# Kernel tuning notes

Hardware: AMD Instinct MI355X
Metric: run time of the kernel (lower is better)

The kernel has to match this reference:

```python
import jax, jax.numpy as jnp
import numpy as np

NUM_LAYERS, B, S, H = 2, 32, 4096, 1024
NEG_INF = -1.0e9


def setup_inputs() -> dict:
    key = jax.random.key(0)
    k1, k2, k3 = jax.random.split(key, 3)
    hidden = jax.random.normal(k1, (NUM_LAYERS, B, H), dtype=jnp.float32)
    encoder_outputs = jax.random.normal(k2, (B, S, H), dtype=jnp.float32)
    mask = jax.random.randint(k3, (B, S), 0, 2).astype(jnp.bool_)
    return {"hidden": hidden, "encoder_outputs": encoder_outputs, "mask": mask}


def reference(hidden, encoder_outputs, mask):
    # hidden: [L, B, H] -> take last layer [B, H]
    h = hidden[-1]
    # scores: [B, S] = einsum over H
    scores = jnp.einsum("bsh,bh->bs", encoder_outputs, h)
    scores = jnp.where(mask, scores, NEG_INF)
    attn = jax.nn.softmax(scores, axis=1)  # [B, S]
    # context: [B, H]
    context = jnp.einsum("bs,bsh->bh", attn, encoder_outputs)
    return (context, attn)
```

## Files before the change

kernel.cpp:

```cpp
#include <hip/hip_runtime.h>
#include <math.h>

#define B_ 32
#define S_ 4096
#define H_ 1024
#define NBLK 16
#define ROWS_PER_BLOCK (S_ / NBLK)
#define NWAVE 4
#define ROWS_PER_WAVE (ROWS_PER_BLOCK / NWAVE)
#define NEG_INF_ -1.0e9f

__global__ __launch_bounds__(256) void attn_pass1(
    const float* __restrict__ hidden,
    const float* __restrict__ enc,
    const int*   __restrict__ mask,
    float* __restrict__ scores,
    float* __restrict__ part_ctx,
    float* __restrict__ part_ml)
{
    const int blk  = blockIdx.x;
    const int b    = blk / NBLK;
    const int cb   = blk % NBLK;
    const int tid  = threadIdx.x;
    const int wave = tid >> 6;
    const int lane = tid & 63;

    const float4* h4 = (const float4*)(hidden + (size_t)(B_ + b) * H_);
    const float4 hf0 = h4[lane];
    const float4 hf1 = h4[lane + 64];
    const float4 hf2 = h4[lane + 128];
    const float4 hf3 = h4[lane + 192];

    float m = -INFINITY;
    float l = 0.0f;
    float4 c0 = {0.f, 0.f, 0.f, 0.f};
    float4 c1 = c0, c2 = c0, c3 = c0;
    float myscore = 0.0f;

    const int    row0  = cb * ROWS_PER_BLOCK + wave * ROWS_PER_WAVE;
    const float* encb  = enc  + (size_t)b * S_ * H_;
    const int*   maskb = mask + (size_t)b * S_;

    for (int r = 0; r < ROWS_PER_WAVE; ++r) {
        const int s = row0 + r;
        const float4* row4 = (const float4*)(encb + (size_t)s * H_);
        const float4 r0 = row4[lane];
        const float4 r1 = row4[lane + 64];
        const float4 r2 = row4[lane + 128];
        const float4 r3 = row4[lane + 192];

        float dot = r0.x * hf0.x + r0.y * hf0.y + r0.z * hf0.z + r0.w * hf0.w;
        dot += r1.x * hf1.x + r1.y * hf1.y + r1.z * hf1.z + r1.w * hf1.w;
        dot += r2.x * hf2.x + r2.y * hf2.y + r2.z * hf2.z + r2.w * hf2.w;
        dot += r3.x * hf3.x + r3.y * hf3.y + r3.z * hf3.z + r3.w * hf3.w;

        #pragma unroll
        for (int off = 32; off >= 1; off >>= 1)
            dot += __shfl_xor(dot, off, 64);

        const float score = (maskb[s] != 0) ? dot : NEG_INF_;
        if (r == lane) myscore = score;

        const float newm  = fmaxf(m, score);
        const float scale = __expf(m - newm);
        const float p     = __expf(score - newm);
        l = l * scale + p;
        c0.x = c0.x * scale + p * r0.x;  c0.y = c0.y * scale + p * r0.y;
        c0.z = c0.z * scale + p * r0.z;  c0.w = c0.w * scale + p * r0.w;
        c1.x = c1.x * scale + p * r1.x;  c1.y = c1.y * scale + p * r1.y;
        c1.z = c1.z * scale + p * r1.z;  c1.w = c1.w * scale + p * r1.w;
        c2.x = c2.x * scale + p * r2.x;  c2.y = c2.y * scale + p * r2.y;
        c2.z = c2.z * scale + p * r2.z;  c2.w = c2.w * scale + p * r2.w;
        c3.x = c3.x * scale + p * r3.x;  c3.y = c3.y * scale + p * r3.y;
        c3.z = c3.z * scale + p * r3.z;  c3.w = c3.w * scale + p * r3.w;
        m = newm;
    }

    scores[(size_t)b * S_ + row0 + lane] = myscore;

    __shared__ float lds_ctx[NWAVE][H_];
    __shared__ float lds_m[NWAVE];
    __shared__ float lds_l[NWAVE];
    float4* dst = (float4*)lds_ctx[wave];
    dst[lane]       = c0;
    dst[lane + 64]  = c1;
    dst[lane + 128] = c2;
    dst[lane + 192] = c3;
    if (lane == 0) { lds_m[wave] = m; lds_l[wave] = l; }
    __syncthreads();

    const float M  = fmaxf(fmaxf(lds_m[0], lds_m[1]), fmaxf(lds_m[2], lds_m[3]));
    const float w0 = __expf(lds_m[0] - M);
    const float w1 = __expf(lds_m[1] - M);
    const float w2 = __expf(lds_m[2] - M);
    const float w3 = __expf(lds_m[3] - M);

    const int e = tid * 4;
    const float4 a0 = *(const float4*)&lds_ctx[0][e];
    const float4 a1 = *(const float4*)&lds_ctx[1][e];
    const float4 a2 = *(const float4*)&lds_ctx[2][e];
    const float4 a3 = *(const float4*)&lds_ctx[3][e];
    float4 o;
    o.x = a0.x * w0 + a1.x * w1 + a2.x * w2 + a3.x * w3;
    o.y = a0.y * w0 + a1.y * w1 + a2.y * w2 + a3.y * w3;
    o.z = a0.z * w0 + a1.z * w1 + a2.z * w2 + a3.z * w3;
    o.w = a0.w * w0 + a1.w * w1 + a2.w * w2 + a3.w * w3;
    *(float4*)&part_ctx[(size_t)blk * H_ + e] = o;

    if (tid == 0) {
        const float L = lds_l[0] * w0 + lds_l[1] * w1 + lds_l[2] * w2 + lds_l[3] * w3;
        part_ml[blk * 2]     = M;
        part_ml[blk * 2 + 1] = L;
    }
}

__global__ __launch_bounds__(256) void attn_pass2(
    const float* __restrict__ part_ctx,
    const float* __restrict__ part_ml,
    float* __restrict__ out_ctx,
    float* __restrict__ attn)
{
    const int b    = blockIdx.x;
    const int part = blockIdx.y;
    const int tid  = threadIdx.x;

    float M = -INFINITY;
    #pragma unroll
    for (int p = 0; p < NBLK; ++p)
        M = fmaxf(M, part_ml[(b * NBLK + p) * 2]);

    float w[NBLK];
    float L = 0.0f;
    #pragma unroll
    for (int p = 0; p < NBLK; ++p) {
        w[p] = __expf(part_ml[(b * NBLK + p) * 2] - M);
        L += part_ml[(b * NBLK + p) * 2 + 1] * w[p];
    }
    const float invL = 1.0f / L;

    if (part == 0) {
        const int e = tid * 4;
        float4 acc = {0.f, 0.f, 0.f, 0.f};
        #pragma unroll
        for (int p = 0; p < NBLK; ++p) {
            const float4 v = *(const float4*)&part_ctx[(size_t)(b * NBLK + p) * H_ + e];
            acc.x += v.x * w[p];  acc.y += v.y * w[p];
            acc.z += v.z * w[p];  acc.w += v.w * w[p];
        }
        acc.x *= invL; acc.y *= invL; acc.z *= invL; acc.w *= invL;
        *(float4*)&out_ctx[(size_t)b * H_ + e] = acc;
    } else {
        const size_t s0 = (size_t)b * S_ + (size_t)(part - 1) * 1024 + tid * 4;
        float4 sc = *(const float4*)&attn[s0];
        sc.x = __expf(sc.x - M) * invL;
        sc.y = __expf(sc.y - M) * invL;
        sc.z = __expf(sc.z - M) * invL;
        sc.w = __expf(sc.w - M) * invL;
        *(float4*)&attn[s0] = sc;
    }
}

extern "C" void kernel_launch(void* const* d_in, const int* in_sizes, int n_in,
                              void* d_out, int out_size, void* d_ws, size_t ws_size,
                              hipStream_t stream) {
    (void)in_sizes; (void)n_in; (void)out_size; (void)ws_size;
    const float* hidden = (const float*)d_in[0];
    const float* enc    = (const float*)d_in[1];
    const int*   mask   = (const int*)d_in[2];

    float* out      = (float*)d_out;
    float* out_ctx  = out;
    float* attn     = out + (size_t)B_ * H_;

    float* part_ctx = (float*)d_ws;
    float* part_ml  = part_ctx + (size_t)B_ * NBLK * H_;

    attn_pass1<<<dim3(B_ * NBLK), dim3(256), 0, stream>>>(
        hidden, enc, mask, attn, part_ctx, part_ml);
    attn_pass2<<<dim3(B_, 5), dim3(256), 0, stream>>>(
        part_ctx, part_ml, out_ctx, attn);
}
```

Before: 686.8 us.

## Process encoder rows in chunks of four and double block count

```diff
diff --git a/kernel.cpp b/kernel.cpp
--- a/kernel.cpp
+++ b/kernel.cpp
@@ -4,13 +4,15 @@
 #define B_ 32
 #define S_ 4096
 #define H_ 1024
-#define NBLK 16
+#define NBLK 32
 #define ROWS_PER_BLOCK (S_ / NBLK)
 #define NWAVE 4
 #define ROWS_PER_WAVE (ROWS_PER_BLOCK / NWAVE)
+#define CHUNK 4
+#define NCHUNK (ROWS_PER_WAVE / CHUNK)
 #define NEG_INF_ -1.0e9f
 
-__global__ __launch_bounds__(256) void attn_pass1(
+__global__ __launch_bounds__(256, 4) void attn_pass1(
     const float* __restrict__ hidden,
     const float* __restrict__ enc,
     const int*   __restrict__ mask,
@@ -19,8 +21,8 @@
     float* __restrict__ part_ml)
 {
     const int blk  = blockIdx.x;
-    const int b    = blk / NBLK;
-    const int cb   = blk % NBLK;
+    const int b    = blk >> 5;
+    const int cb   = blk & 31;
     const int tid  = threadIdx.x;
     const int wave = tid >> 6;
     const int lane = tid & 63;
@@ -41,42 +43,72 @@
     const float* encb  = enc  + (size_t)b * S_ * H_;
     const int*   maskb = mask + (size_t)b * S_;
 
-    for (int r = 0; r < ROWS_PER_WAVE; ++r) {
-        const int s = row0 + r;
-        const float4* row4 = (const float4*)(encb + (size_t)s * H_);
-        const float4 r0 = row4[lane];
-        const float4 r1 = row4[lane + 64];
-        const float4 r2 = row4[lane + 128];
-        const float4 r3 = row4[lane + 192];
-
-        float dot = r0.x * hf0.x + r0.y * hf0.y + r0.z * hf0.z + r0.w * hf0.w;
-        dot += r1.x * hf1.x + r1.y * hf1.y + r1.z * hf1.z + r1.w * hf1.w;
-        dot += r2.x * hf2.x + r2.y * hf2.y + r2.z * hf2.z + r2.w * hf2.w;
-        dot += r3.x * hf3.x + r3.y * hf3.y + r3.z * hf3.z + r3.w * hf3.w;
-
-        #pragma unroll
-        for (int off = 32; off >= 1; off >>= 1)
-            dot += __shfl_xor(dot, off, 64);
-
-        const float score = (maskb[s] != 0) ? dot : NEG_INF_;
-        if (r == lane) myscore = score;
-
-        const float newm  = fmaxf(m, score);
+    for (int k = 0; k < NCHUNK; ++k) {
+        const int sbase = row0 + k * CHUNK;
+
+        float4 r[CHUNK][4];
+        #pragma unroll
+        for (int c = 0; c < CHUNK; ++c) {
+            const float4* row4 = (const float4*)(encb + (size_t)(sbase + c) * H_);
+            r[c][0] = row4[lane];
+            r[c][1] = row4[lane + 64];
+            r[c][2] = row4[lane + 128];
+            r[c][3] = row4[lane + 192];
+        }
+
+        float pd[CHUNK];
+        #pragma unroll
+        for (int c = 0; c < CHUNK; ++c) {
+            float d = r[c][0].x * hf0.x + r[c][0].y * hf0.y + r[c][0].z * hf0.z + r[c][0].w * hf0.w;
+            d += r[c][1].x * hf1.x + r[c][1].y * hf1.y + r[c][1].z * hf1.z + r[c][1].w * hf1.w;
+            d += r[c][2].x * hf2.x + r[c][2].y * hf2.y + r[c][2].z * hf2.z + r[c][2].w * hf2.w;
+            d += r[c][3].x * hf3.x + r[c][3].y * hf3.y + r[c][3].z * hf3.z + r[c][3].w * hf3.w;
+            pd[c] = d;
+        }
+
+        #pragma unroll
+        for (int off = 32; off >= 1; off >>= 1) {
+            #pragma unroll
+            for (int c = 0; c < CHUNK; ++c)
+                pd[c] += __shfl_xor(pd[c], off, 64);
+        }
+
+        float sc[CHUNK];
+        #pragma unroll
+        for (int c = 0; c < CHUNK; ++c) {
+            sc[c] = (maskb[sbase + c] != 0) ? pd[c] : NEG_INF_;
+            if (lane == k * CHUNK + c) myscore = sc[c];
+        }
+
+        float cmax = fmaxf(fmaxf(sc[0], sc[1]), fmaxf(sc[2], sc[3]));
+        const float newm  = fmaxf(m, cmax);
         const float scale = __expf(m - newm);
-        const float p     = __expf(score - newm);
-        l = l * scale + p;
-        c0.x = c0.x * scale + p * r0.x;  c0.y = c0.y * scale + p * r0.y;
-        c0.z = c0.z * scale + p * r0.z;  c0.w = c0.w * scale + p * r0.w;
-        c1.x = c1.x * scale + p * r1.x;  c1.y = c1.y * scale + p * r1.y;
-        c1.z = c1.z * scale + p * r1.z;  c1.w = c1.w * scale + p * r1.w;
-        c2.x = c2.x * scale + p * r2.x;  c2.y = c2.y * scale + p * r2.y;
-        c2.z = c2.z * scale + p * r2.z;  c2.w = c2.w * scale + p * r2.w;
-        c3.x = c3.x * scale + p * r3.x;  c3.y = c3.y * scale + p * r3.y;
-        c3.z = c3.z * scale + p * r3.z;  c3.w = c3.w * scale + p * r3.w;
+        float p[CHUNK];
+        float psum = 0.0f;
+        #pragma unroll
+        for (int c = 0; c < CHUNK; ++c) { p[c] = __expf(sc[c] - newm); psum += p[c]; }
+        l = l * scale + psum;
+
+        c0.x *= scale; c0.y *= scale; c0.z *= scale; c0.w *= scale;
+        c1.x *= scale; c1.y *= scale; c1.z *= scale; c1.w *= scale;
+        c2.x *= scale; c2.y *= scale; c2.z *= scale; c2.w *= scale;
+        c3.x *= scale; c3.y *= scale; c3.z *= scale; c3.w *= scale;
+        #pragma unroll
+        for (int c = 0; c < CHUNK; ++c) {
+            c0.x += p[c] * r[c][0].x;  c0.y += p[c] * r[c][0].y;
+            c0.z += p[c] * r[c][0].z;  c0.w += p[c] * r[c][0].w;
+            c1.x += p[c] * r[c][1].x;  c1.y += p[c] * r[c][1].y;
+            c1.z += p[c] * r[c][1].z;  c1.w += p[c] * r[c][1].w;
+            c2.x += p[c] * r[c][2].x;  c2.y += p[c] * r[c][2].y;
+            c2.z += p[c] * r[c][2].z;  c2.w += p[c] * r[c][2].w;
+            c3.x += p[c] * r[c][3].x;  c3.y += p[c] * r[c][3].y;
+            c3.z += p[c] * r[c][3].z;  c3.w += p[c] * r[c][3].w;
+        }
         m = newm;
     }
 
-    scores[(size_t)b * S_ + row0 + lane] = myscore;
+    if (lane < ROWS_PER_WAVE)
+        scores[(size_t)b * S_ + row0 + lane] = myscore;
 
     __shared__ float lds_ctx[NWAVE][H_];
     __shared__ float lds_m[NWAVE];
@@ -129,8 +161,8 @@
     for (int p = 0; p < NBLK; ++p)
         M = fmaxf(M, part_ml[(b * NBLK + p) * 2]);
 
+    float L = 0.0f;
     float w[NBLK];
-    float L = 0.0f;
     #pragma unroll
     for (int p = 0; p < NBLK; ++p) {
         w[p] = __expf(part_ml[(b * NBLK + p) * 2] - M);
```

New measurement: 693.2 us. No clear change (+0.9%).
